# Kernel tuning notes

Hardware: AMD Instinct MI355X
Metric: run time of the kernel (lower is better)

## Reference

```python
import jax, jax.numpy as jnp
import numpy as np

B, T, D = 2, 2048, 2048
N_HEAD, N_KV_HEAD = 16, 4
HEAD_DIM = D // N_HEAD  # 128
N_REP = N_HEAD // N_KV_HEAD  # 4
ROPE_THETA = 10000.0
EPS = float(jnp.finfo(jnp.float32).eps)  # torch.nn.RMSNorm default eps


def setup_inputs() -> dict:
    key = jax.random.key(0)
    ks = jax.random.split(key, 6)
    s = 0.02
    return {
        "x": jax.random.normal(ks[0], (B, T, D), jnp.float32),
        "wq": jax.random.normal(ks[1], (N_HEAD * HEAD_DIM, D), jnp.float32) * s,
        "wk": jax.random.normal(ks[2], (N_KV_HEAD * HEAD_DIM, D), jnp.float32) * s,
        "wv": jax.random.normal(ks[3], (N_KV_HEAD * HEAD_DIM, D), jnp.float32) * s,
        "wo": jax.random.normal(ks[4], (D, D), jnp.float32) * s,
        "q_norm_w": jnp.ones((HEAD_DIM,), jnp.float32),
        "k_norm_w": jnp.ones((HEAD_DIM,), jnp.float32),
    }


def _rope(x):
    # x: (B, T, H, hd). Llama/Qwen complex-pair RoPE on consecutive pairs.
    t = x.shape[1]
    hd = x.shape[-1]
    inv_freq = 1.0 / (ROPE_THETA ** (jnp.arange(0, hd, 2, dtype=jnp.float32) / hd))
    ang = jnp.arange(t, dtype=jnp.float32)[:, None] * inv_freq[None, :]  # (T, hd/2)
    cos = jnp.cos(ang)[None, :, None, :]
    sin = jnp.sin(ang)[None, :, None, :]
    xr = x[..., 0::2]
    xi = x[..., 1::2]
    or_ = xr * cos - xi * sin
    oi_ = xr * sin + xi * cos
    return jnp.stack([or_, oi_], axis=-1).reshape(x.shape)


def _rmsnorm(x, w):
    var = jnp.mean(jnp.square(x), axis=-1, keepdims=True)
    return x * jax.lax.rsqrt(var + EPS) * w


def reference(x, wq, wk, wv, wo, q_norm_w, k_norm_w):
    b, t, d = x.shape
    xq = (x @ wq.T).reshape(b, t, N_HEAD, HEAD_DIM)
    xk = (x @ wk.T).reshape(b, t, N_KV_HEAD, HEAD_DIM)
    xv = (x @ wv.T).reshape(b, t, N_KV_HEAD, HEAD_DIM)
    xq = _rope(xq)
    xk = _rope(xk)
    # repeat_kv: (B,T,KV,hd) -> (B,T,KV*n_rep,hd)
    xk = jnp.repeat(xk, N_REP, axis=2)
    xv = jnp.repeat(xv, N_REP, axis=2)
    # (B, H, T, hd)
    xq = xq.transpose(0, 2, 1, 3)
    xk = xk.transpose(0, 2, 1, 3)
    xv = xv.transpose(0, 2, 1, 3)
    xq = _rmsnorm(xq, q_norm_w)
    xk = _rmsnorm(xk, k_norm_w)
    scale = 1.0 / np.sqrt(HEAD_DIM)
    scores = jnp.einsum("bhqd,bhkd->bhqk", xq, xk) * scale
    causal = jnp.tril(jnp.ones((t, t), bool))
    scores = jnp.where(causal[None, None], scores, -jnp.inf)
    attn = jax.nn.softmax(scores, axis=-1)
    y = jnp.einsum("bhqk,bhkd->bhqd", attn, xv)
    y = y.transpose(0, 2, 1, 3).reshape(b, t, d)
    return y @ wo.T
```

## Files before the change

### kernel.cpp

```cpp
#include <hip/hip_runtime.h>
#include <hip/hip_bf16.h>
#include <math.h>

typedef __attribute__((ext_vector_type(8))) short bf16x8;
typedef __attribute__((ext_vector_type(4))) float f32x4;
typedef __attribute__((ext_vector_type(4))) unsigned int u32x4;
typedef __attribute__((ext_vector_type(2))) unsigned int u32x2;

#define DEV static __device__ __forceinline__

constexpr int TT   = 2048;
constexpr int DDIM = 2048;
constexpr int QKVN = 3072;
constexpr int MROWS = 4096;
constexpr float RSCALE = 0.08838834764831845f;
constexpr float LOG2E  = 1.4426950408889634f;
constexpr float SC2    = RSCALE * LOG2E;
constexpr float REPS   = 1.1920928955078125e-07f;

DEV unsigned short f2b(float f) {
  union { float f; unsigned int u; } v; v.f = f;
  unsigned int u = v.u;
  return (unsigned short)((u + 0x7fffu + ((u >> 16) & 1u)) >> 16);
}
DEV float b2f(unsigned short h) {
  union { unsigned int u; float f; } v; v.u = ((unsigned int)h) << 16;
  return v.f;
}
DEV f32x4 mfma16(bf16x8 a, bf16x8 b, f32x4 c) {
  return __builtin_amdgcn_mfma_f32_16x16x32_bf16(a, b, c, 0, 0, 0);
}
DEV void gload_lds16(const void* g, void* l) {
  __builtin_amdgcn_global_load_lds(
      (const __attribute__((address_space(1))) unsigned int*)g,
      (__attribute__((address_space(3))) unsigned int*)l, 16, 0, 0);
}
DEV unsigned int cvtpk(float lo, float hi) {
  unsigned int r;
  asm("v_cvt_pk_bf16_f32 %0, %1, %2" : "=v"(r) : "v"(lo), "v"(hi));
  return r;
}
union PB { u32x4 u; bf16x8 b; };

__global__ __launch_bounds__(256) void cvt_kernel(const float* __restrict__ in,
                                                  unsigned short* __restrict__ out,
                                                  int n4) {
  int i = blockIdx.x * 256 + threadIdx.x;
  if (i < n4) {
    float4 v = ((const float4*)in)[i];
    ushort4 o;
    o.x = f2b(v.x); o.y = f2b(v.y); o.z = f2b(v.z); o.w = f2b(v.w);
    ((ushort4*)out)[i] = o;
  }
}

template <typename CT>
__global__ __launch_bounds__(256) void gemm_bt(const unsigned short* __restrict__ A,
                                               const unsigned short* __restrict__ B,
                                               CT* __restrict__ C,
                                               int M, int N, int K) {
  __shared__ unsigned short As[2][128 * 32];
  __shared__ unsigned short Bs[2][128 * 32];
  const int tid = threadIdx.x;
  const int l = tid & 63, w = tid >> 6;
  const int wr = w >> 1, wc = w & 1;
  const long bm = (long)blockIdx.y * 128, bn = (long)blockIdx.x * 128;

  const int r0 = tid >> 2;
  const int c0 = (tid & 3) * 8;
  const unsigned short* Ag0 = A + (bm + r0) * (long)K + c0;
  const unsigned short* Ag1 = A + (bm + r0 + 64) * (long)K + c0;
  const unsigned short* Bg0 = B + (bn + r0) * (long)K + c0;
  const unsigned short* Bg1 = B + (bn + r0 + 64) * (long)K + c0;

  f32x4 acc[4][4];
#pragma unroll
  for (int m = 0; m < 4; ++m)
#pragma unroll
    for (int n = 0; n < 4; ++n) acc[m][n] = f32x4{0.f, 0.f, 0.f, 0.f};

  const int lr = l & 15;
  const int lk = (l >> 4) * 8;

  {
    char* lA = (char*)(As[0]) + w * 1024;
    char* lB = (char*)(Bs[0]) + w * 1024;
    gload_lds16(Ag0, lA);
    gload_lds16(Ag1, lA + 4096);
    gload_lds16(Bg0, lB);
    gload_lds16(Bg1, lB + 4096);
  }
  __syncthreads();

  int cur = 0;
  for (int k0 = 0; k0 < K; k0 += 32) {
    if (k0 + 32 < K) {
      char* lA = (char*)(As[cur ^ 1]) + w * 1024;
      char* lB = (char*)(Bs[cur ^ 1]) + w * 1024;
      gload_lds16(Ag0 + k0 + 32, lA);
      gload_lds16(Ag1 + k0 + 32, lA + 4096);
      gload_lds16(Bg0 + k0 + 32, lB);
      gload_lds16(Bg1 + k0 + 32, lB + 4096);
    }
    const unsigned short* Asc = As[cur];
    const unsigned short* Bsc = Bs[cur];
    bf16x8 af[4], bfr[4];
#pragma unroll
    for (int m = 0; m < 4; ++m)
      af[m] = *(const bf16x8*)(Asc + (wr * 64 + m * 16 + lr) * 32 + lk);
#pragma unroll
    for (int n = 0; n < 4; ++n)
      bfr[n] = *(const bf16x8*)(Bsc + (wc * 64 + n * 16 + lr) * 32 + lk);
#pragma unroll
    for (int m = 0; m < 4; ++m)
#pragma unroll
      for (int n = 0; n < 4; ++n)
        acc[m][n] = mfma16(af[m], bfr[n], acc[m][n]);
    __syncthreads();
    cur ^= 1;
  }

#pragma unroll
  for (int m = 0; m < 4; ++m)
#pragma unroll
    for (int n = 0; n < 4; ++n)
#pragma unroll
      for (int r = 0; r < 4; ++r) {
        long row = bm + wr * 64 + m * 16 + (l >> 4) * 4 + r;
        long col = bn + wc * 64 + n * 16 + (l & 15);
        float val = acc[m][n][r];
        if constexpr (sizeof(CT) == 2)
          ((unsigned short*)C)[row * N + col] = f2b(val);
        else
          ((float*)C)[row * N + col] = val;
      }
}

__global__ __launch_bounds__(256) void rope_norm_kernel(unsigned short* __restrict__ qkv,
                                                        const float* __restrict__ qw,
                                                        const float* __restrict__ kw) {
  const int slot = blockIdx.x * 4 + (threadIdx.x >> 6);
  const int l = threadIdx.x & 63;
  const int bt = slot / 20;
  const int hs = slot - bt * 20;
  const int t = bt & (TT - 1);
  const bool isq = hs < 16;
  const int col0 = isq ? hs * 128 : 2048 + (hs - 16) * 128;
  const float* w = isq ? qw : kw;
  unsigned short* p = qkv + (long)bt * QKVN + col0;

  unsigned int pr = *(const unsigned int*)(p + 2 * l);
  float xr = b2f((unsigned short)(pr & 0xffffu));
  float xi = b2f((unsigned short)(pr >> 16));

  float ang = (float)t * exp2f(-0.207620509f * (float)l);
  float s = sinf(ang), c = cosf(ang);
  float orr = xr * c - xi * s;
  float oii = xr * s + xi * c;

  float ss = orr * orr + oii * oii;
#pragma unroll
  for (int d = 1; d < 64; d <<= 1) ss += __shfl_xor(ss, d);
  float sc = rsqrtf(ss * (1.f / 128.f) + REPS);

  unsigned int outw = ((unsigned int)f2b(oii * sc * w[2 * l + 1]) << 16) |
                      (unsigned int)f2b(orr * sc * w[2 * l]);
  *(unsigned int*)(p + 2 * l) = outw;
}

__global__ __launch_bounds__(256) void fattn_kernel(const unsigned short* __restrict__ qkv,
                                                    unsigned short* __restrict__ y) {
  const int bx = blockIdx.x;
  const int bh = blockIdx.y;
  const int b = bh >> 4, h = bh & 15;
  const unsigned short* base = qkv + (long)b * TT * QKVN;
  const unsigned short* Qp = base + h * 128;
  const unsigned short* Kp = base + 2048 + (h >> 2) * 128;
  const unsigned short* Vp = base + 2560 + (h >> 2) * 128;
  const int tid = threadIdx.x;
  const int l = tid & 63, w = tid >> 6;
  const int lr = l & 15, lg = l >> 4;

  __shared__ char KsB[2][16384];
  __shared__ char VtB[2][16384];

  const int krow0 = tid >> 4;
  const int kcolb = ((tid & 15) * 16) ^ ((krow0 & 7) << 4);
  const unsigned short* Kg = Kp + (long)krow0 * QKVN + (kcolb >> 1);
  const int vm = tid & 15;
  const unsigned short* Vg = Vp + (long)(tid >> 4) * QKVN + vm * 8;
  const int lgk = ((lr & 7) << 4);

  for (int seg = 0; seg < 2; ++seg) {
    const int qb = seg ? bx : (31 - bx);
    const int qrow = qb * 64 + w * 16;
    const int ntiles = qb + 1;

    bf16x8 qf[4];
    {
      const unsigned short* qp = Qp + (long)(qrow + lr) * QKVN + lg * 8;
#pragma unroll
      for (int c = 0; c < 4; ++c) qf[c] = *(const bf16x8*)(qp + c * 32);
    }

    f32x4 o[8];
#pragma unroll
    for (int n = 0; n < 8; ++n) o[n] = f32x4{0.f, 0.f, 0.f, 0.f};
    float m = -__builtin_inff(), lsum = 0.f;

    __syncthreads();

    u32x4 vr[4];
    {
      char* kdst = KsB[0] + (w * 64) * 16;
#pragma unroll
      for (int i = 0; i < 4; ++i)
        gload_lds16(Kg + (long)16 * i * QKVN, kdst + i * 4096);
#pragma unroll
      for (int i = 0; i < 4; ++i)
        vr[i] = *(const u32x4*)(Vg + (long)16 * i * QKVN);
      asm volatile("s_waitcnt vmcnt(0)" ::: "memory");
      char* vt = VtB[0];
#pragma unroll
      for (int i = 0; i < 4; ++i) {
        int kv2 = 2 * ((tid >> 4) + 16 * i);
        const unsigned short* tv = (const unsigned short*)&vr[i];
#pragma unroll
        for (int j = 0; j < 8; ++j) {
          int d = vm * 8 + j;
          int swz = (((d >> 1) ^ (d >> 3)) & 7) << 4;
          *(unsigned short*)(vt + d * 128 + (kv2 ^ swz)) = tv[j];
        }
      }
      asm volatile("s_waitcnt lgkmcnt(0)" ::: "memory");
      __builtin_amdgcn_sched_barrier(0);
      __builtin_amdgcn_s_barrier();
    }

    int cur = 0;
    for (int it = 0; it < ntiles; ++it) {
      const int kv0 = it * 64;
      const int nxt = cur ^ 1;
      const bool pfn = (it + 1 < ntiles);

      if (pfn) {
        const long adv = (long)(it + 1) * 64 * QKVN;
        char* kdst = KsB[nxt] + (w * 64) * 16;
#pragma unroll
        for (int i = 0; i < 4; ++i)
          gload_lds16(Kg + adv + (long)16 * i * QKVN, kdst + i * 4096);
#pragma unroll
        for (int i = 0; i < 4; ++i)
          vr[i] = *(const u32x4*)(Vg + adv + (long)16 * i * QKVN);
      }

      const char* KsC = KsB[cur];
      const char* VtC = VtB[cur];

      f32x4 sT[4];
      __builtin_amdgcn_s_setprio(1);
#pragma unroll
      for (int kb = 0; kb < 4; ++kb) {
        if (kv0 + kb * 16 <= qrow + 15) {
          f32x4 s = f32x4{0.f, 0.f, 0.f, 0.f};
#pragma unroll
          for (int c = 0; c < 4; ++c) {
            bf16x8 kf = *(const bf16x8*)(KsC + (kb * 16 + lr) * 256 +
                                         ((16 * lg + 64 * c) ^ lgk));
            s = mfma16(kf, qf[c], s);
          }
          sT[kb] = s;
        } else {
          sT[kb] = f32x4{-__builtin_inff(), -__builtin_inff(),
                         -__builtin_inff(), -__builtin_inff()};
        }
      }
      __builtin_amdgcn_s_setprio(0);

      if (kv0 + 48 >= qrow) {
#pragma unroll
        for (int kb = 0; kb < 4; ++kb)
#pragma unroll
          for (int r = 0; r < 4; ++r) {
            int ks = kv0 + kb * 16 + 4 * lg + r;
            sT[kb][r] = (ks > qrow + lr) ? -__builtin_inff() : sT[kb][r];
          }
      }

      float pmax = -__builtin_inff();
#pragma unroll
      for (int kb = 0; kb < 4; ++kb)
#pragma unroll
        for (int r = 0; r < 4; ++r) pmax = fmaxf(pmax, sT[kb][r]);
      pmax = fmaxf(pmax, __shfl_xor(pmax, 16));
      pmax = fmaxf(pmax, __shfl_xor(pmax, 32));
      pmax *= SC2;

      if (!__all(pmax <= m + 8.f)) {
        float mn = fmaxf(m, pmax);
        float al = exp2f(m - mn);
        m = mn;
        lsum *= al;
        float ao[4];
#pragma unroll
        for (int r = 0; r < 4; ++r) ao[r] = __shfl(al, 20 * lg + r);
#pragma unroll
        for (int n = 0; n < 8; ++n)
#pragma unroll
          for (int r = 0; r < 4; ++r) o[n][r] *= ao[r];
      }

      float rs = 0.f;
      unsigned int pk[4][2];
#pragma unroll
      for (int kb = 0; kb < 4; ++kb) {
        float p0 = exp2f(sT[kb][0] * SC2 - m);
        float p1 = exp2f(sT[kb][1] * SC2 - m);
        float p2 = exp2f(sT[kb][2] * SC2 - m);
        float p3 = exp2f(sT[kb][3] * SC2 - m);
        rs += (p0 + p1) + (p2 + p3);
        pk[kb][0] = cvtpk(p0, p1);
        pk[kb][1] = cvtpk(p2, p3);
      }
      rs += __shfl_xor(rs, 16);
      rs += __shfl_xor(rs, 32);
      lsum += rs;

      __builtin_amdgcn_s_setprio(1);
#pragma unroll
      for (int c = 0; c < 2; ++c) {
        if (kv0 + c * 32 <= qrow + 15) {
          PB pb;
          pb.u = u32x4{pk[2 * c][0], pk[2 * c][1], pk[2 * c + 1][0], pk[2 * c + 1][1]};
#pragma unroll
          for (int n = 0; n < 8; ++n) {
            int d = n * 16 + lr;
            int gsw = (((d >> 1) ^ (d >> 3)) & 7) << 4;
            const char* vb = VtC + d * 128;
            u32x2 vlo = *(const u32x2*)(vb + ((64 * c + 8 * lg) ^ gsw));
            u32x2 vhi = *(const u32x2*)(vb + ((64 * c + 32 + 8 * lg) ^ gsw));
            PB vv; vv.u = u32x4{vlo[0], vlo[1], vhi[0], vhi[1]};
            o[n] = mfma16(pb.b, vv.b, o[n]);
          }
        }
      }
      __builtin_amdgcn_s_setprio(0);

      if (pfn) {
        asm volatile("s_waitcnt vmcnt(0)" ::: "memory");
        char* vt = VtB[nxt];
#pragma unroll
        for (int i = 0; i < 4; ++i) {
          int kv2 = 2 * ((tid >> 4) + 16 * i);
          const unsigned short* tv = (const unsigned short*)&vr[i];
#pragma unroll
          for (int j = 0; j < 8; ++j) {
            int d = vm * 8 + j;
            int swz = (((d >> 1) ^ (d >> 3)) & 7) << 4;
            *(unsigned short*)(vt + d * 128 + (kv2 ^ swz)) = tv[j];
          }
        }
        asm volatile("s_waitcnt lgkmcnt(0)" ::: "memory");
        __builtin_amdgcn_sched_barrier(0);
        __builtin_amdgcn_s_barrier();
      }
      cur = nxt;
    }

    float inv = 1.f / lsum;
    float io[4];
#pragma unroll
    for (int r = 0; r < 4; ++r) io[r] = __shfl(inv, 20 * lg + r);
    unsigned short* yp = y + (long)(b * TT + qrow) * DDIM + h * 128;
#pragma unroll
    for (int n = 0; n < 8; ++n)
#pragma unroll
      for (int r = 0; r < 4; ++r)
        yp[(long)(lg * 4 + r) * DDIM + n * 16 + lr] = f2b(o[n][r] * io[r]);
  }
}

extern "C" void kernel_launch(void* const* d_in, const int* in_sizes, int n_in,
                              void* d_out, int out_size, void* d_ws, size_t ws_size,
                              hipStream_t stream) {
  const float* x  = (const float*)d_in[0];
  const float* wq = (const float*)d_in[1];
  const float* wk = (const float*)d_in[2];
  const float* wv = (const float*)d_in[3];
  const float* wo = (const float*)d_in[4];
  const float* qw = (const float*)d_in[5];
  const float* kw = (const float*)d_in[6];
  float* out = (float*)d_out;

  unsigned short* xb   = (unsigned short*)d_ws;
  unsigned short* wcat = xb + (size_t)MROWS * DDIM;
  unsigned short* wob  = wcat + (size_t)QKVN * DDIM;
  unsigned short* qkv  = wob + (size_t)DDIM * DDIM;
  unsigned short* yb   = qkv + (size_t)MROWS * QKVN;

  auto cvt = [&](const float* src, unsigned short* dst, long n) {
    int n4 = (int)(n / 4);
    cvt_kernel<<<(n4 + 255) / 256, 256, 0, stream>>>(src, dst, n4);
  };
  cvt(x,  xb,   (long)MROWS * DDIM);
  cvt(wq, wcat,                         (long)2048 * 2048);
  cvt(wk, wcat + (size_t)2048 * 2048,   (long)512 * 2048);
  cvt(wv, wcat + (size_t)2560 * 2048,   (long)512 * 2048);
  cvt(wo, wob,  (long)2048 * 2048);

  dim3 g1(QKVN / 128, MROWS / 128);
  gemm_bt<unsigned short><<<g1, 256, 0, stream>>>(xb, wcat, qkv, MROWS, QKVN, DDIM);

  rope_norm_kernel<<<(MROWS * 20) / 4, 256, 0, stream>>>(qkv, qw, kw);

  dim3 g2(16, 32);
  fattn_kernel<<<g2, 256, 0, stream>>>(qkv, yb);

  dim3 g3(DDIM / 128, MROWS / 128);
  gemm_bt<float><<<g3, 256, 0, stream>>>(yb, wob, out, MROWS, DDIM, DDIM);
}
```

Baseline: 421.1 us.

## Replace GEMM with 256x256-tile 8-wave kernel using swizzled LDS and staged prefetch

Replaces the 128x128 double-buffered GEMM with a 256x256-tile, 512-thread kernel over a K=64 step. It uses 128KB of dynamic LDS, XOR-swizzled LDS layout, interleaved quarter-tile prefetch, s_setprio around MFMA bursts and an XCD-aware block remap. The goal is more data reuse per LDS load, fewer bank conflicts and global loads overlapped with compute. The cost is only 192 and 128 workgroups, which can leave CUs idle on a 256-CU device, plus heavy register and LDS pressure.

New measurement: 450.7 us. 7.0% more time.

```diff
diff --git a/kernel.cpp b/kernel.cpp
--- a/kernel.cpp
+++ b/kernel.cpp
@@ -55,80 +55,151 @@
 }
 
 template <typename CT>
-__global__ __launch_bounds__(256) void gemm_bt(const unsigned short* __restrict__ A,
-                                               const unsigned short* __restrict__ B,
-                                               CT* __restrict__ C,
-                                               int M, int N, int K) {
-  __shared__ unsigned short As[2][128 * 32];
-  __shared__ unsigned short Bs[2][128 * 32];
+__global__ __launch_bounds__(512, 2) void gemm256_bt(const unsigned short* __restrict__ A,
+                                                     const unsigned short* __restrict__ B,
+                                                     CT* __restrict__ C,
+                                                     int N, int K, int nbx, int nwg) {
+  extern __shared__ char smem[];
   const int tid = threadIdx.x;
   const int l = tid & 63, w = tid >> 6;
-  const int wr = w >> 1, wc = w & 1;
-  const long bm = (long)blockIdx.y * 128, bn = (long)blockIdx.x * 128;
-
-  const int r0 = tid >> 2;
-  const int c0 = (tid & 3) * 8;
-  const unsigned short* Ag0 = A + (bm + r0) * (long)K + c0;
-  const unsigned short* Ag1 = A + (bm + r0 + 64) * (long)K + c0;
-  const unsigned short* Bg0 = B + (bn + r0) * (long)K + c0;
-  const unsigned short* Bg1 = B + (bn + r0 + 64) * (long)K + c0;
-
-  f32x4 acc[4][4];
-#pragma unroll
-  for (int m = 0; m < 4; ++m)
-#pragma unroll
-    for (int n = 0; n < 4; ++n) acc[m][n] = f32x4{0.f, 0.f, 0.f, 0.f};
-
-  const int lr = l & 15;
-  const int lk = (l >> 4) * 8;
-
-  {
-    char* lA = (char*)(As[0]) + w * 1024;
-    char* lB = (char*)(Bs[0]) + w * 1024;
-    gload_lds16(Ag0, lA);
-    gload_lds16(Ag1, lA + 4096);
-    gload_lds16(Bg0, lB);
-    gload_lds16(Bg1, lB + 4096);
+  const int lr = l & 15, lg = l >> 4;
+  const int wm = w >> 2, wn = w & 3;
+
+  const int cpx = nwg >> 3;
+  const int sbid = ((int)blockIdx.x % 8) * cpx + (int)blockIdx.x / 8;
+  const int bx = sbid % nbx, by = sbid / nbx;
+
+  const int colb = ((l & 7) * 16) ^ (((l >> 5) & 1) << 5);
+  const unsigned short* Asrc = A + (long)(by * 256 + w * 8 + (l >> 3)) * K + (colb >> 1);
+  const unsigned short* Bsrc = B + (long)(bx * 256 + w * 8 + (l >> 3)) * K + (colb >> 1);
+  const int ldst_w = w * 1024;
+
+  auto STAGE = [&](int ht, int t) {
+    const unsigned short* s0 = (ht < 2 ? Asrc : Bsrc) + (long)((ht & 1) * 128) * K + t * 64;
+    char* d0 = smem + ((t & 1) * 65536 + ht * 16384 + ldst_w);
+    gload_lds16(s0, d0);
+    gload_lds16(s0 + (long)64 * K, d0 + 8192);
+  };
+
+  const int swz_r = (lr & 4) << 3;
+  auto LDA = [&](int db, int mi, int kk) -> bf16x8 {
+    return *(const bf16x8*)(smem + db * 65536 + wm * 16384 +
+                            (mi * 16 + lr) * 128 + ((kk * 64 + lg * 16) ^ swz_r));
+  };
+  auto LDB = [&](int db, int ni, int kk) -> bf16x8 {
+    return *(const bf16x8*)(smem + db * 65536 + 32768 + (wn >> 1) * 16384 +
+                            ((wn & 1) * 64 + ni * 16 + lr) * 128 +
+                            ((kk * 64 + lg * 16) ^ swz_r));
+  };
+
+  f32x4 acc[8][4];
+#pragma unroll
+  for (int mi = 0; mi < 8; ++mi)
+#pragma unroll
+    for (int ni = 0; ni < 4; ++ni) acc[mi][ni] = f32x4{0.f, 0.f, 0.f, 0.f};
+
+  const int NT = K >> 6;
+
+  STAGE(0, 0); STAGE(1, 0); STAGE(2, 0); STAGE(3, 0); STAGE(0, 1);
+  asm volatile("s_waitcnt vmcnt(2)" ::: "memory");
+  __builtin_amdgcn_s_barrier();
+
+  for (int u = 0; u < NT; ++u) {
+    const int db = u & 1;
+    bf16x8 af[4][2], bfr[2][2];
+
+#pragma unroll
+    for (int mi = 0; mi < 4; ++mi) { af[mi][0] = LDA(db, mi, 0); af[mi][1] = LDA(db, mi, 1); }
+#pragma unroll
+    for (int ni = 0; ni < 2; ++ni) { bfr[ni][0] = LDB(db, ni, 0); bfr[ni][1] = LDB(db, ni, 1); }
+    if (u + 1 < NT) STAGE(1, u + 1);
+    asm volatile("s_waitcnt lgkmcnt(8)" ::: "memory");
+    __builtin_amdgcn_s_barrier();
+    asm volatile("s_waitcnt lgkmcnt(0)" ::: "memory");
+    __builtin_amdgcn_sched_barrier(0);
+    __builtin_amdgcn_s_setprio(1);
+#pragma unroll
+    for (int mi = 0; mi < 4; ++mi)
+#pragma unroll
+      for (int ni = 0; ni < 2; ++ni) {
+        acc[mi][ni] = mfma16(af[mi][0], bfr[ni][0], acc[mi][ni]);
+        acc[mi][ni] = mfma16(af[mi][1], bfr[ni][1], acc[mi][ni]);
+      }
+    __builtin_amdgcn_s_setprio(0);
+    __builtin_amdgcn_sched_barrier(0);
+    __builtin_amdgcn_s_barrier();
+
+#pragma unroll
+    for (int ni = 0; ni < 2; ++ni) { bfr[ni][0] = LDB(db, ni + 2, 0); bfr[ni][1] = LDB(db, ni + 2, 1); }
+    if (u + 1 < NT) STAGE(2, u + 1);
+    __builtin_amdgcn_s_barrier();
+    asm volatile("s_waitcnt lgkmcnt(0)" ::: "memory");
+    __builtin_amdgcn_sched_barrier(0);
+    __builtin_amdgcn_s_setprio(1);
+#pragma unroll
+    for (int mi = 0; mi < 4; ++mi)
+#pragma unroll
+      for (int ni = 0; ni < 2; ++ni) {
+        acc[mi][ni + 2] = mfma16(af[mi][0], bfr[ni][0], acc[mi][ni + 2]);
+        acc[mi][ni + 2] = mfma16(af[mi][1], bfr[ni][1], acc[mi][ni + 2]);
+      }
+    __builtin_amdgcn_s_setprio(0);
+    __builtin_amdgcn_sched_barrier(0);
+    __builtin_amdgcn_s_barrier();
+
+#pragma unroll
+    for (int mi = 0; mi < 4; ++mi) { af[mi][0] = LDA(db, mi + 4, 0); af[mi][1] = LDA(db, mi + 4, 1); }
+    if (u + 1 < NT) STAGE(3, u + 1);
+    __builtin_amdgcn_s_barrier();
+    asm volatile("s_waitcnt lgkmcnt(0)" ::: "memory");
+    __builtin_amdgcn_sched_barrier(0);
+    __builtin_amdgcn_s_setprio(1);
+#pragma unroll
+    for (int mi = 0; mi < 4; ++mi)
+#pragma unroll
+      for (int ni = 0; ni < 2; ++ni) {
+        acc[mi + 4][ni + 2] = mfma16(af[mi][0], bfr[ni][0], acc[mi + 4][ni + 2]);
+        acc[mi + 4][ni + 2] = mfma16(af[mi][1], bfr[ni][1], acc[mi + 4][ni + 2]);
+      }
+    __builtin_amdgcn_s_setprio(0);
+    __builtin_amdgcn_sched_barrier(0);
+    __builtin_amdgcn_s_barrier();
+
+#pragma unroll
+    for (int ni = 0; ni < 2; ++ni) { bfr[ni][0] = LDB(db, ni, 0); bfr[ni][1] = LDB(db, ni, 1); }
+    if (u + 2 < NT) STAGE(0, u + 2);
+    __builtin_amdgcn_s_barrier();
+    asm volatile("s_waitcnt lgkmcnt(0)" ::: "memory");
+    __builtin_amdgcn_sched_barrier(0);
+    __builtin_amdgcn_s_setprio(1);
+#pragma unroll
+    for (int mi = 0; mi < 4; ++mi)
+#pragma unroll
+      for (int ni = 0; ni < 2; ++ni) {
+        acc[mi + 4][ni] = mfma16(af[mi][0], bfr[ni][0], acc[mi + 4][ni]);
+        acc[mi + 4][ni] = mfma16(af[mi][1], bfr[ni][1], acc[mi + 4][ni]);
+      }
+    __builtin_amdgcn_s_setprio(0);
+    __builtin_amdgcn_sched_barrier(0);
+    if (u + 2 < NT) {
+      asm volatile("s_waitcnt vmcnt(2)" ::: "memory");
+    } else {
+      asm volatile("s_waitcnt vmcnt(0)" ::: "memory");
+    }
+    __builtin_amdgcn_s_barrier();
   }
-  __syncthreads();
-
-  int cur = 0;
-  for (int k0 = 0; k0 < K; k0 += 32) {
-    if (k0 + 32 < K) {
-      char* lA = (char*)(As[cur ^ 1]) + w * 1024;
-      char* lB = (char*)(Bs[cur ^ 1]) + w * 1024;
-      gload_lds16(Ag0 + k0 + 32, lA);
-      gload_lds16(Ag1 + k0 + 32, lA + 4096);
-      gload_lds16(Bg0 + k0 + 32, lB);
-      gload_lds16(Bg1 + k0 + 32, lB + 4096);
-    }
-    const unsigned short* Asc = As[cur];
-    const unsigned short* Bsc = Bs[cur];
-    bf16x8 af[4], bfr[4];
-#pragma unroll
-    for (int m = 0; m < 4; ++m)
-      af[m] = *(const bf16x8*)(Asc + (wr * 64 + m * 16 + lr) * 32 + lk);
-#pragma unroll
-    for (int n = 0; n < 4; ++n)
-      bfr[n] = *(const bf16x8*)(Bsc + (wc * 64 + n * 16 + lr) * 32 + lk);
-#pragma unroll
-    for (int m = 0; m < 4; ++m)
-#pragma unroll
-      for (int n = 0; n < 4; ++n)
-        acc[m][n] = mfma16(af[m], bfr[n], acc[m][n]);
-    __syncthreads();
-    cur ^= 1;
-  }
-
-#pragma unroll
-  for (int m = 0; m < 4; ++m)
-#pragma unroll
-    for (int n = 0; n < 4; ++n)
+
+  const long crow0 = (long)by * 256 + wm * 128 + lg * 4;
+  const long ccol0 = (long)bx * 256 + wn * 64 + lr;
+#pragma unroll
+  for (int mi = 0; mi < 8; ++mi)
+#pragma unroll
+    for (int ni = 0; ni < 4; ++ni)
 #pragma unroll
       for (int r = 0; r < 4; ++r) {
-        long row = bm + wr * 64 + m * 16 + (l >> 4) * 4 + r;
-        long col = bn + wc * 64 + n * 16 + (l & 15);
-        float val = acc[m][n][r];
+        long row = crow0 + mi * 16 + r;
+        long col = ccol0 + ni * 16;
+        float val = acc[mi][ni][r];
         if constexpr (sizeof(CT) == 2)
           ((unsigned short*)C)[row * N + col] = f2b(val);
         else
@@ -398,6 +469,11 @@
   unsigned short* qkv  = wob + (size_t)DDIM * DDIM;
   unsigned short* yb   = qkv + (size_t)MROWS * QKVN;
 
+  (void)hipFuncSetAttribute((const void*)gemm256_bt<unsigned short>,
+                            hipFuncAttributeMaxDynamicSharedMemorySize, 131072);
+  (void)hipFuncSetAttribute((const void*)gemm256_bt<float>,
+                            hipFuncAttributeMaxDynamicSharedMemorySize, 131072);
+
   auto cvt = [&](const float* src, unsigned short* dst, long n) {
     int n4 = (int)(n / 4);
     cvt_kernel<<<(n4 + 255) / 256, 256, 0, stream>>>(src, dst, n4);
@@ -408,14 +484,14 @@
   cvt(wv, wcat + (size_t)2560 * 2048,   (long)512 * 2048);
   cvt(wo, wob,  (long)2048 * 2048);
 
-  dim3 g1(QKVN / 128, MROWS / 128);
-  gemm_bt<unsigned short><<<g1, 256, 0, stream>>>(xb, wcat, qkv, MROWS, QKVN, DDIM);
+  gemm256_bt<unsigned short><<<dim3(192), dim3(512), 131072, stream>>>(
+      xb, wcat, qkv, QKVN, DDIM, 12, 192);
 
   rope_norm_kernel<<<(MROWS * 20) / 4, 256, 0, stream>>>(qkv, qw, kw);
 
   dim3 g2(16, 32);
   fattn_kernel<<<g2, 256, 0, stream>>>(qkv, yb);
 
-  dim3 g3(DDIM / 128, MROWS / 128);
-  gemm_bt<float><<<g3, 256, 0, stream>>>(yb, wob, out, MROWS, DDIM, DDIM);
-}
+  gemm256_bt<float><<<dim3(128), dim3(512), 131072, stream>>>(
+      yb, wob, out, DDIM, DDIM, 8, 128);
+}
```
